# Kernel optimization log

Measured on AMD Instinct MI355X. Metric: run time of the kernel, lower is better.

## Reference

```python
import jax, jax.numpy as jnp
import numpy as np

N = 50000
E = 800000
D = 256        # encoder_dim; also hidden*heads for both layers
H = 4          # heads
C = 64         # hidden_dim per head
OUT = 5        # classes
NEG_SLOPE = 0.2
GN_EPS = 1e-5
SM_EPS = 1e-16  # PyG softmax denominator epsilon


def setup_inputs() -> dict:
    key = jax.random.key(0)
    ks = jax.random.split(key, 20)
    sc = lambda fan_in: 1.0 / np.sqrt(fan_in)
    inp = {
        "x": jax.random.normal(ks[0], (N, D), dtype=jnp.float32),
        "edge_index": jax.random.randint(ks[1], (2, E), 0, N, dtype=jnp.int64),
        # two GATv2 layers (stacked on leading axis): lin_l, lin_r, att, bias
        "Wl": jax.random.normal(ks[2], (2, D, H * C), dtype=jnp.float32) * sc(D),
        "Wr": jax.random.normal(ks[3], (2, D, H * C), dtype=jnp.float32) * sc(D),
        "att": jax.random.normal(ks[4], (2, H, C), dtype=jnp.float32) * sc(C),
        "bconv": jnp.zeros((2, H * C), dtype=jnp.float32),
        # parallel linear skips
        "Wlin": jax.random.normal(ks[5], (2, D, H * C), dtype=jnp.float32) * sc(D),
        "blin": jnp.zeros((2, H * C), dtype=jnp.float32),
        # GraphNorm params
        "gn_w": jnp.ones((2, H * C), dtype=jnp.float32),
        "gn_b": jnp.zeros((2, H * C), dtype=jnp.float32),
        "gn_ms": jnp.ones((2, H * C), dtype=jnp.float32),
        # final GATv2 (concat=False -> head mean, out=5) and final linear
        "fWl": jax.random.normal(ks[6], (D, H * OUT), dtype=jnp.float32) * sc(D),
        "fWr": jax.random.normal(ks[7], (D, H * OUT), dtype=jnp.float32) * sc(D),
        "fatt": jax.random.normal(ks[8], (H, OUT), dtype=jnp.float32) * sc(OUT),
        "fbconv": jnp.zeros((OUT,), dtype=jnp.float32),
        "fWlin": jax.random.normal(ks[9], (D, OUT), dtype=jnp.float32) * sc(D),
        "fblin": jnp.zeros((OUT,), dtype=jnp.float32),
    }
    return inp


def _gatv2(x, src, dst, Wl, Wr, att, heads, ch):
    # x: [N, Din]; returns [N, heads, ch]
    n = x.shape[0]
    xl = (x @ Wl).reshape(n, heads, ch)  # source messages
    xr = (x @ Wr).reshape(n, heads, ch)  # target query part
    e = jax.nn.leaky_relu(xl[src] + xr[dst], NEG_SLOPE)      # [E, H, C]
    score = jnp.einsum("ehc,hc->eh", e, att)                  # [E, H]
    # segment softmax over incoming edges of each target node
    m = jax.ops.segment_max(score, dst, num_segments=n)       # [N, H]
    a = jnp.exp(score - m[dst])
    denom = jax.ops.segment_sum(a, dst, num_segments=n)       # [N, H]
    alpha = a / (denom[dst] + SM_EPS)                         # [E, H]
    return jax.ops.segment_sum(alpha[..., None] * xl[src], dst, num_segments=n)


def _graphnorm(x, w, b, ms):
    mean = jnp.mean(x, axis=0)
    centered = x - mean * ms
    var = jnp.mean(centered * centered, axis=0)
    return w * centered * jax.lax.rsqrt(var + GN_EPS) + b


def reference(x, edge_index, Wl, Wr, att, bconv, Wlin, blin, gn_w, gn_b, gn_ms,
              fWl, fWr, fatt, fbconv, fWlin, fblin):
    src, dst = edge_index[0], edge_index[1]
    emb = x
    for i in range(2):
        cpart = _gatv2(emb, src, dst, Wl[i], Wr[i], att[i], H, C).reshape(N, H * C) + bconv[i]
        lpart = emb @ Wlin[i] + blin[i]
        cpart = _graphnorm(cpart, gn_w[i], gn_b[i], gn_ms[i])
        emb = jax.nn.elu(cpart + lpart)
    cpart = _gatv2(emb, src, dst, fWl, fWr, fatt, H, OUT).mean(axis=1) + fbconv  # concat=False
    lpart = emb @ fWlin + fblin
    return jax.nn.log_softmax(cpart + lpart, axis=1)
```

## Files before the change

kernel.cpp:

```cpp
#include <hip/hip_runtime.h>

#define NN 50000
#define EE 800000
#define DD 256
#define NB 196

typedef unsigned short u16;
typedef unsigned int u32;

typedef __attribute__((ext_vector_type(8))) short short8;
typedef __attribute__((ext_vector_type(4))) float f32x4;
typedef __attribute__((ext_vector_type(4))) unsigned short u16x4;

__device__ __forceinline__ float b2f(u16 u) {
  union { u32 i; float f; } c; c.i = ((u32)u) << 16; return c.f;
}
__device__ __forceinline__ u16 f2b(float f) {
  union { float f; u32 i; } c; c.f = f;
  u32 u = c.i;
  return (u16)((u + 0x7fffu + ((u >> 16) & 1u)) >> 16);
}
__device__ __forceinline__ float lrelu(float x) { return x > 0.f ? x : 0.2f * x; }
__device__ __forceinline__ float ldf(const void* p, int i, int bf) {
  return bf ? b2f(((const u16*)p)[i]) : ((const float*)p)[i];
}
__device__ __forceinline__ int lde(const void* ei, int idx, int m64) {
  int v = m64 ? (int)((const long long*)ei)[idx] : ((const int*)ei)[idx];
  return v < 0 ? 0 : (v >= NN ? NN - 1 : v);
}
__device__ __forceinline__ float cexp(float s) {
  return __expf(fminf(fmaxf(s, -60.f), 60.f));
}

__global__ __launch_bounds__(256) void init_kernel(const void* x, const void* ei,
                                                   int* flags, int* cnt) {
  int i = blockIdx.x * 256 + threadIdx.x;
  if (i < NN) cnt[i] = 0;
  if (blockIdx.x == 0 && threadIdx.x < 64) {
    int lane = threadIdx.x;
    const u16* xw = (const u16*)x;
    int c = 0;
    for (int k = lane; k < 512; k += 64) {
      u16 w = xw[k];
      int e = (w >> 7) & 0xFF;
      if ((e >= 107 && e <= 147) || (w & 0x7FFF) == 0) ++c;
    }
    const u32* ew = (const u32*)ei;
    int zc = 0;
    for (int k = 1 + 2 * lane; k < 1024; k += 128)
      if (ew[k] == 0) ++zc;
    #pragma unroll
    for (int off = 1; off < 64; off <<= 1) {
      c += __shfl_xor(c, off);
      zc += __shfl_xor(zc, off);
    }
    if (lane == 0) {
      flags[0] = (c >= 440) ? 1 : 0;
      flags[1] = (zc >= 400) ? 1 : 0;
    }
  }
}

__global__ void hist_kernel(const void* ei, const int* flags, int* cnt) {
  int e = blockIdx.x * 256 + threadIdx.x;
  if (e < EE) atomicAdd(&cnt[lde(ei, EE + e, flags[1])], 1);
}

__global__ __launch_bounds__(256) void bsum_kernel(const int* __restrict__ deg,
                                                   int* __restrict__ bsum) {
  int i = blockIdx.x * 256 + threadIdx.x;
  int v = (i < NN) ? deg[i] : 0;
  #pragma unroll
  for (int off = 1; off < 64; off <<= 1) v += __shfl_xor(v, off);
  __shared__ int ws[4];
  int lane = threadIdx.x & 63, wid = threadIdx.x >> 6;
  if (lane == 0) ws[wid] = v;
  __syncthreads();
  if (threadIdx.x == 0) bsum[blockIdx.x] = ws[0] + ws[1] + ws[2] + ws[3];
}

__global__ __launch_bounds__(256) void bscan_kernel(const int* __restrict__ bsum,
                                                    int* __restrict__ boff) {
  int t = threadIdx.x;
  int v = (t < NB) ? bsum[t] : 0;
  int iv = v;
  int lane = t & 63, wid = t >> 6;
  #pragma unroll
  for (int off = 1; off < 64; off <<= 1) {
    int u = __shfl_up(iv, off);
    if (lane >= off) iv += u;
  }
  __shared__ int ws[4];
  if (lane == 63) ws[wid] = iv;
  __syncthreads();
  int add = 0;
  for (int w = 0; w < wid; ++w) add += ws[w];
  if (t < NB) boff[t] = iv - v + add;
}

__global__ __launch_bounds__(256) void bwrite_kernel(const int* __restrict__ deg,
                                                     const int* __restrict__ boff,
                                                     int* __restrict__ rowptr) {
  int i = blockIdx.x * 256 + threadIdx.x;
  int v = (i < NN) ? deg[i] : 0;
  int iv = v;
  int lane = threadIdx.x & 63, wid = threadIdx.x >> 6;
  #pragma unroll
  for (int off = 1; off < 64; off <<= 1) {
    int u = __shfl_up(iv, off);
    if (lane >= off) iv += u;
  }
  __shared__ int ws[4];
  if (lane == 63) ws[wid] = iv;
  __syncthreads();
  int add = boff[blockIdx.x];
  for (int w = 0; w < wid; ++w) add += ws[w];
  if (i <= NN) rowptr[i] = iv - v + add;
}

__global__ void fill_kernel(const void* ei, const int* flags, const int* __restrict__ rowptr,
                            int* __restrict__ cnt, int* __restrict__ col) {
  int e = blockIdx.x * 256 + threadIdx.x;
  if (e < EE) {
    int m64 = flags[1];
    int dst = lde(ei, EE + e, m64);
    int old = atomicSub(&cnt[dst], 1);
    int pos = rowptr[dst] + old - 1;
    if (pos >= 0 && pos < EE) col[pos] = lde(ei, e, m64);
  }
}

__global__ __launch_bounds__(256) void prep_kernel(
    const void* Wl, const void* Wr, const void* Wlin,
    const void* fWl, const void* fWr, const void* fWlin,
    const void* x, const int* flags, u16* wpack, u16* fwp, u16* xb) {
  int bf = flags[0];
  int bid = blockIdx.x;
  if (bid < 1536) {
    int idx = bid * 256 + threadIdx.x;
    int m = idx >> 16, e = idx & 65535;
    int layer = (m >= 3) ? 1 : 0, sel = m - layer * 3;
    const void* src = (sel == 0 ? Wl : (sel == 1 ? Wr : Wlin));
    int k = e >> 8, n = e & 255;
    wpack[(m << 16) + ((((k >> 3) << 8) + n) << 3) + (k & 7)] =
        f2b(ldf(src, layer * 65536 + e, bf));
  } else if (bid < 1584) {
    int idx = (bid - 1536) * 256 + threadIdx.x;
    int j = idx & 7;
    int col = (idx >> 3) % 48;
    int kk = idx / (48 * 8);
    int k = kk * 8 + j;
    float v = 0.f;
    if (col < 20)      v = ldf(fWl, k * 20 + col, bf);
    else if (col < 40) v = ldf(fWr, k * 20 + (col - 20), bf);
    else if (col < 45) v = ldf(fWlin, k * 5 + (col - 40), bf);
    fwp[idx] = f2b(v);
  } else {
    int base = (bid - 1584) * 1024 + threadIdx.x * 4;
    if (bf) {
      const u16* s = (const u16*)x;
      #pragma unroll
      for (int j = 0; j < 4; ++j) xb[base + j] = s[base + j];
    } else {
      const float* s = (const float*)x;
      #pragma unroll
      for (int j = 0; j < 4; ++j) xb[base + j] = f2b(s[base + j]);
    }
  }
}

__global__ __launch_bounds__(256) void gemm_kernel(
    const u16* __restrict__ A, const u16* __restrict__ wpack, const void* blin,
    const int* flags, int layer, float* __restrict__ sums,
    u16* __restrict__ xl, u16* __restrict__ xr, u16* __restrict__ lp, int M) {
  __shared__ __align__(16) u16 bsh[16384];
  if (blockIdx.x == 0 && blockIdx.y == 0) {
    sums[threadIdx.x] = 0.f;
    sums[threadIdx.x + 256] = 0.f;
  }
  int wave = threadIdx.x >> 6;
  int lane = threadIdx.x & 63;
  int q = lane >> 4;
  int t = lane & 15;
  int m0 = blockIdx.x * 64 + wave * 16;
  int yh = blockIdx.y;

  int arow = m0 + t;
  if (arow >= M) arow = M - 1;
  const u16* Abase = A + (size_t)arow * DD + q * 8;
  short8 af[8];
  #pragma unroll
  for (int i = 0; i < 8; ++i) af[i] = *(const short8*)(Abase + i * 32);

  int bf = flags[0];

  for (int yi = 0; yi < 6; ++yi) {
    int y = yh * 6 + yi;
    int m = y >> 2;
    int col0 = (y & 3) * 64;
    const u16* wb = wpack + (m << 16);

    __syncthreads();
    #pragma unroll
    for (int itc = 0; itc < 8; ++itc) {
      int chunk = threadIdx.x + itc * 256;
      int kk = chunk >> 6;
      int off = chunk & 63;
      *(uint4*)&bsh[(kk << 9) + (off << 3)] =
          *(const uint4*)(wb + (((kk << 8) + col0) << 3) + (off << 3));
    }
    __syncthreads();

    f32x4 acc[4];
    #pragma unroll
    for (int ns = 0; ns < 4; ++ns) acc[ns] = (f32x4){0.f, 0.f, 0.f, 0.f};

    #pragma unroll
    for (int i = 0; i < 8; ++i) {
      int kk = i * 4 + q;
      const u16* bb = &bsh[(kk << 9) + (t << 3)];
      #pragma unroll
      for (int ns = 0; ns < 4; ++ns) {
        short8 b = *(const short8*)(bb + (ns << 7));
        acc[ns] = __builtin_amdgcn_mfma_f32_16x16x32_bf16(af[i], b, acc[ns], 0, 0, 0);
      }
    }

    u16* dstp = (y < 4) ? xl : (y < 8) ? xr : lp;
    bool isLp = (y >= 8);
    #pragma unroll
    for (int ns = 0; ns < 4; ++ns) {
      int c = col0 + ns * 16 + t;
      float bias = isLp ? ldf(blin, layer * 256 + c, bf) : 0.f;
      #pragma unroll
      for (int r = 0; r < 4; ++r) {
        int row = m0 + q * 4 + r;
        if (row < M) dstp[(size_t)row * DD + c] = f2b(acc[ns][r] + bias);
      }
    }
  }
}

__global__ __launch_bounds__(256) void fgemm_kernel(
    const u16* __restrict__ A, const u16* __restrict__ fwp, const void* fblin,
    const int* flags, float* __restrict__ zl, float* __restrict__ zr,
    float* __restrict__ lp5, int M) {
  int wave = threadIdx.x >> 6;
  int lane = threadIdx.x & 63;
  int q = lane >> 4;
  int t = lane & 15;
  int m0 = blockIdx.x * 64 + wave * 16;

  f32x4 acc[3];
  #pragma unroll
  for (int ns = 0; ns < 3; ++ns) acc[ns] = (f32x4){0.f, 0.f, 0.f, 0.f};

  int arow = m0 + t;
  if (arow >= M) arow = M - 1;
  const u16* Abase = A + (size_t)arow * DD + q * 8;

  #pragma unroll
  for (int k0 = 0; k0 < DD; k0 += 32) {
    short8 a = *(const short8*)(Abase + k0);
    int kk = (k0 >> 3) + q;
    #pragma unroll
    for (int ns = 0; ns < 3; ++ns) {
      short8 b = *(const short8*)(fwp + (((kk * 48) + ns * 16 + t) << 3));
      acc[ns] = __builtin_amdgcn_mfma_f32_16x16x32_bf16(a, b, acc[ns], 0, 0, 0);
    }
  }

  int bf = flags[0];
  #pragma unroll
  for (int ns = 0; ns < 3; ++ns) {
    int c = ns * 16 + t;
    #pragma unroll
    for (int r = 0; r < 4; ++r) {
      int row = m0 + q * 4 + r;
      if (row < M) {
        float v = acc[ns][r];
        if (c < 20)      zl[row * 20 + c] = v;
        else if (c < 40) zr[row * 20 + (c - 20)] = v;
        else if (c < 45) lp5[row * 5 + (c - 40)] = v + ldf(fblin, c - 40, bf);
      }
    }
  }
}

__global__ __launch_bounds__(64) void agg_kernel(
    const u16* __restrict__ xl, const u16* __restrict__ xr,
    const int* __restrict__ rowptr, const int* __restrict__ col,
    const void* att, const void* bconv, const int* flags, int layer,
    u16* __restrict__ cpart) {
  int node = blockIdx.x;
  int lane = threadIdx.x;
  int h = lane >> 4;
  int cb = (lane & 15) * 4;
  int base = h * 64 + cb;
  int bf = flags[0];

  u16x4 r4 = *(const u16x4*)(xr + (size_t)node * DD + base);
  float xrv[4], atv[4];
  #pragma unroll
  for (int j = 0; j < 4; ++j) {
    xrv[j] = b2f(r4[j]);
    atv[j] = ldf(att, layer * 256 + base + j, bf);
  }

  float l = 0.f;
  float acc[4] = {0.f, 0.f, 0.f, 0.f};
  int e0 = rowptr[node], e1 = rowptr[node + 1];
  for (int e = e0; e < e1; ++e) {
    int src = col[e];
    u16x4 s4 = *(const u16x4*)(xl + (size_t)src * DD + base);
    float x0 = b2f(s4[0]), x1 = b2f(s4[1]), x2 = b2f(s4[2]), x3 = b2f(s4[3]);
    float sp = atv[0] * lrelu(x0 + xrv[0]) + atv[1] * lrelu(x1 + xrv[1]) +
               atv[2] * lrelu(x2 + xrv[2]) + atv[3] * lrelu(x3 + xrv[3]);
    sp += __shfl_xor(sp, 1);
    sp += __shfl_xor(sp, 2);
    sp += __shfl_xor(sp, 4);
    sp += __shfl_xor(sp, 8);
    float pz = cexp(sp);
    l += pz;
    acc[0] += pz * x0;
    acc[1] += pz * x1;
    acc[2] += pz * x2;
    acc[3] += pz * x3;
  }
  float inv = 1.f / (l + 1e-16f);
  u16x4 outw;
  #pragma unroll
  for (int j = 0; j < 4; ++j)
    outw[j] = f2b(acc[j] * inv + ldf(bconv, layer * 256 + base + j, bf));
  *(u16x4*)(cpart + (size_t)node * DD + base) = outw;
}

__global__ __launch_bounds__(256) void stats_kernel(const u16* __restrict__ cpart,
                                                    float* __restrict__ sums) {
  int ch = threadIdx.x;
  int n0 = blockIdx.x * 250, n1 = n0 + 250;
  float s = 0.f, s2 = 0.f;
  for (int n = n0; n < n1; ++n) {
    float x = b2f(cpart[(size_t)n * DD + ch]);
    s += x; s2 += x * x;
  }
  atomicAdd(&sums[ch], s);
  atomicAdd(&sums[256 + ch], s2);
}

__global__ __launch_bounds__(256) void norm_kernel(
    const u16* __restrict__ cpart, const u16* __restrict__ lp,
    const void* gw, const void* gb, const void* gms, const int* flags, int layer,
    const float* __restrict__ sums, u16* __restrict__ emb) {
  int node = blockIdx.x, ch = threadIdx.x;
  int bf = flags[0];
  size_t idx = (size_t)node * DD + ch;
  const float invN = 1.f / (float)NN;
  float mean = sums[ch] * invN;
  float ex2 = sums[256 + ch] * invN;
  float mm = mean * ldf(gms, layer * 256 + ch, bf);
  float var = ex2 - 2.f * mm * mean + mm * mm;
  float x = b2f(cpart[idx]);
  float y = ldf(gw, layer * 256 + ch, bf) * (x - mm) * rsqrtf(fmaxf(var, 0.f) + 1e-5f) +
            ldf(gb, layer * 256 + ch, bf) + b2f(lp[idx]);
  emb[idx] = f2b(y > 0.f ? y : expm1f(y));
}

__global__ __launch_bounds__(64) void finagg_kernel(
    const float* __restrict__ zl, const float* __restrict__ zr,
    const int* __restrict__ rowptr, const int* __restrict__ col,
    const void* fatt, const void* fbconv, const int* flags,
    const float* __restrict__ lp5, void* outv) {
  int node = blockIdx.x, lane = threadIdx.x;
  int bf = flags[0];
  int h = lane >> 4, sub = lane & 15;

  float zrv[5], atv[5];
  #pragma unroll
  for (int c = 0; c < 5; ++c) {
    zrv[c] = zr[node * 20 + h * 5 + c];
    atv[c] = ldf(fatt, h * 5 + c, bf);
  }
  float l = 0.f, acc[5] = {0.f, 0.f, 0.f, 0.f, 0.f};
  int e0 = rowptr[node], e1 = rowptr[node + 1];
  for (int e = e0 + sub; e < e1; e += 16) {
    int src = col[e];
    const float* zs = zl + src * 20 + h * 5;
    float zlv[5];
    #pragma unroll
    for (int c = 0; c < 5; ++c) zlv[c] = zs[c];
    float s = 0.f;
    #pragma unroll
    for (int c = 0; c < 5; ++c) s += atv[c] * lrelu(zlv[c] + zrv[c]);
    float pz = cexp(s);
    l += pz;
    #pragma unroll
    for (int c = 0; c < 5; ++c) acc[c] += pz * zlv[c];
  }
  #pragma unroll
  for (int off = 1; off < 16; off <<= 1) {
    l += __shfl_xor(l, off);
    #pragma unroll
    for (int c = 0; c < 5; ++c) acc[c] += __shfl_xor(acc[c], off);
  }
  float inv = 1.f / (l + 1e-16f);
  float v[5];
  #pragma unroll
  for (int c = 0; c < 5; ++c) {
    float tv = acc[c] * inv;
    tv += __shfl_xor(tv, 16);
    tv += __shfl_xor(tv, 32);
    v[c] = tv * 0.25f;
  }
  if (lane == 0) {
    float mx = -3.0e38f;
    #pragma unroll
    for (int c = 0; c < 5; ++c) {
      v[c] += ldf(fbconv, c, bf) + lp5[node * 5 + c];
      mx = fmaxf(mx, v[c]);
    }
    float se = 0.f;
    #pragma unroll
    for (int c = 0; c < 5; ++c) se += __expf(v[c] - mx);
    float lse = mx + __logf(se);
    #pragma unroll
    for (int c = 0; c < 5; ++c) {
      float r = v[c] - lse;
      if (bf) ((u16*)outv)[node * 5 + c] = f2b(r);
      else    ((float*)outv)[node * 5 + c] = r;
    }
  }
}

extern "C" void kernel_launch(void* const* d_in, const int* in_sizes, int n_in,
                              void* d_out, int out_size, void* d_ws, size_t ws_size,
                              hipStream_t stream) {
  (void)in_sizes; (void)n_in; (void)out_size; (void)ws_size;
  const void* x     = d_in[0];
  const void* ei    = d_in[1];
  const void* Wl    = d_in[2];
  const void* Wr    = d_in[3];
  const void* att   = d_in[4];
  const void* bconv = d_in[5];
  const void* Wlin  = d_in[6];
  const void* blin  = d_in[7];
  const void* gnw   = d_in[8];
  const void* gnb   = d_in[9];
  const void* gnms  = d_in[10];
  const void* fWl   = d_in[11];
  const void* fWr   = d_in[12];
  const void* fatt  = d_in[13];
  const void* fbc   = d_in[14];
  const void* fWlin = d_in[15];
  const void* fblin = d_in[16];

  char* p = (char*)d_ws;
  auto take = [&](size_t bytes) {
    char* r = p;
    p += (bytes + 511) & ~(size_t)511;
    return r;
  };
  int* flags   = (int*)take(512);
  int* rowptr  = (int*)take((NN + 1) * sizeof(int));
  int* cnt     = (int*)take(NN * sizeof(int));
  int* colx    = (int*)take(EE * sizeof(int));
  int* bsum    = (int*)take(256 * sizeof(int));
  int* boff    = (int*)take(256 * sizeof(int));
  u16* wpack   = (u16*)take((size_t)6 * 65536 * sizeof(u16));
  u16* fwp     = (u16*)take((size_t)32 * 48 * 8 * sizeof(u16));
  float* sums  = (float*)take(512 * sizeof(float));
  char* unionA = take((size_t)NN * DD * 4);
  u16* xb      = (u16*)unionA;
  u16* cpart   = (u16*)unionA;
  float* zl    = (float*)unionA;
  float* zr    = (float*)(unionA + (size_t)NN * 20 * 4);
  float* lp5   = (float*)(unionA + (size_t)NN * 40 * 4);
  u16* xl      = (u16*)take((size_t)NN * DD * 2);
  u16* xr      = (u16*)take((size_t)NN * DD * 2);
  u16* lp      = (u16*)take((size_t)NN * DD * 2);
  u16* emb     = (u16*)take((size_t)NN * DD * 2);

  init_kernel<<<dim3(NB), dim3(256), 0, stream>>>(x, ei, flags, cnt);
  hist_kernel<<<dim3((EE + 255) / 256), dim3(256), 0, stream>>>(ei, flags, cnt);
  bsum_kernel<<<dim3(NB), dim3(256), 0, stream>>>(cnt, bsum);
  bscan_kernel<<<dim3(1), dim3(256), 0, stream>>>(bsum, boff);
  bwrite_kernel<<<dim3(NB), dim3(256), 0, stream>>>(cnt, boff, rowptr);
  fill_kernel<<<dim3((EE + 255) / 256), dim3(256), 0, stream>>>(ei, flags, rowptr, cnt, colx);
  prep_kernel<<<dim3(1584 + NN * DD / 1024), dim3(256), 0, stream>>>(
      Wl, Wr, Wlin, fWl, fWr, fWlin, x, flags, wpack, fwp, xb);

  const u16* layerin = xb;
  for (int i = 0; i < 2; ++i) {
    gemm_kernel<<<dim3((NN + 63) / 64, 2), dim3(256), 0, stream>>>(
        layerin, wpack + (size_t)i * 3 * 65536, blin, flags, i, sums, xl, xr, lp, NN);
    agg_kernel<<<dim3(NN), dim3(64), 0, stream>>>(xl, xr, rowptr, colx, att, bconv,
                                                  flags, i, cpart);
    stats_kernel<<<dim3(200), dim3(256), 0, stream>>>(cpart, sums);
    norm_kernel<<<dim3(NN), dim3(256), 0, stream>>>(cpart, lp, gnw, gnb, gnms, flags, i,
                                                    sums, emb);
    layerin = emb;
  }
  fgemm_kernel<<<dim3((NN + 63) / 64), dim3(256), 0, stream>>>(emb, fwp, fblin, flags,
                                                               zl, zr, lp5, NN);
  finagg_kernel<<<dim3(NN), dim3(64), 0, stream>>>(zl, zr, rowptr, colx, fatt, fbc, flags,
                                                   lp5, d_out);
}
```

Measured before the change: 604.9 us.

## Pack four nodes per block, unroll edge gathers, vectorize norm and prep loads

Aggregation and final-aggregation kernels now run four nodes per 256-thread block instead of one node per 64-thread block. The edge loop is unrolled by four so several gather loads are in flight at once. The norm kernel handles four channels per thread with vector loads and stores, the input conversion in prep uses vector loads, and stats uses more, smaller blocks. lrelu becomes a branch-free fmax. The goal is lower launch and block-scheduling overhead and more memory-level parallelism on the irregular gathers, at the cost of imbalance when nodes in one block have very different degrees.

```diff
diff --git a/kernel.cpp b/kernel.cpp
--- a/kernel.cpp
+++ b/kernel.cpp
@@ -20,7 +20,7 @@
   u32 u = c.i;
   return (u16)((u + 0x7fffu + ((u >> 16) & 1u)) >> 16);
 }
-__device__ __forceinline__ float lrelu(float x) { return x > 0.f ? x : 0.2f * x; }
+__device__ __forceinline__ float lrelu(float x) { return fmaxf(x, 0.2f * x); }
 __device__ __forceinline__ float ldf(const void* p, int i, int bf) {
   return bf ? b2f(((const u16*)p)[i]) : ((const float*)p)[i];
 }
@@ -158,13 +158,13 @@
   } else {
     int base = (bid - 1584) * 1024 + threadIdx.x * 4;
     if (bf) {
-      const u16* s = (const u16*)x;
+      *(u16x4*)(xb + base) = *(const u16x4*)((const u16*)x + base);
+    } else {
+      f32x4 s = *(const f32x4*)((const float*)x + base);
+      u16x4 o;
       #pragma unroll
-      for (int j = 0; j < 4; ++j) xb[base + j] = s[base + j];
-    } else {
-      const float* s = (const float*)x;
-      #pragma unroll
-      for (int j = 0; j < 4; ++j) xb[base + j] = f2b(s[base + j]);
+      for (int j = 0; j < 4; ++j) o[j] = f2b(s[j]);
+      *(u16x4*)(xb + base) = o;
     }
   }
 }
@@ -287,13 +287,31 @@
   }
 }
 
-__global__ __launch_bounds__(64) void agg_kernel(
+__device__ __forceinline__ void edge_step(u16x4 s4, const float* xrv, const float* atv,
+                                          float& l, float* acc) {
+  float x0 = b2f(s4[0]), x1 = b2f(s4[1]), x2 = b2f(s4[2]), x3 = b2f(s4[3]);
+  float sp = atv[0] * lrelu(x0 + xrv[0]) + atv[1] * lrelu(x1 + xrv[1]) +
+             atv[2] * lrelu(x2 + xrv[2]) + atv[3] * lrelu(x3 + xrv[3]);
+  sp += __shfl_xor(sp, 1);
+  sp += __shfl_xor(sp, 2);
+  sp += __shfl_xor(sp, 4);
+  sp += __shfl_xor(sp, 8);
+  float pz = cexp(sp);
+  l += pz;
+  acc[0] += pz * x0;
+  acc[1] += pz * x1;
+  acc[2] += pz * x2;
+  acc[3] += pz * x3;
+}
+
+__global__ __launch_bounds__(256) void agg_kernel(
     const u16* __restrict__ xl, const u16* __restrict__ xr,
     const int* __restrict__ rowptr, const int* __restrict__ col,
     const void* att, const void* bconv, const int* flags, int layer,
     u16* __restrict__ cpart) {
-  int node = blockIdx.x;
-  int lane = threadIdx.x;
+  int wave = threadIdx.x >> 6;
+  int node = blockIdx.x * 4 + wave;
+  int lane = threadIdx.x & 63;
   int h = lane >> 4;
   int cb = (lane & 15) * 4;
   int base = h * 64 + cb;
@@ -310,23 +328,25 @@
   float l = 0.f;
   float acc[4] = {0.f, 0.f, 0.f, 0.f};
   int e0 = rowptr[node], e1 = rowptr[node + 1];
-  for (int e = e0; e < e1; ++e) {
-    int src = col[e];
-    u16x4 s4 = *(const u16x4*)(xl + (size_t)src * DD + base);
-    float x0 = b2f(s4[0]), x1 = b2f(s4[1]), x2 = b2f(s4[2]), x3 = b2f(s4[3]);
-    float sp = atv[0] * lrelu(x0 + xrv[0]) + atv[1] * lrelu(x1 + xrv[1]) +
-               atv[2] * lrelu(x2 + xrv[2]) + atv[3] * lrelu(x3 + xrv[3]);
-    sp += __shfl_xor(sp, 1);
-    sp += __shfl_xor(sp, 2);
-    sp += __shfl_xor(sp, 4);
-    sp += __shfl_xor(sp, 8);
-    float pz = cexp(sp);
-    l += pz;
-    acc[0] += pz * x0;
-    acc[1] += pz * x1;
-    acc[2] += pz * x2;
-    acc[3] += pz * x3;
-  }
+  const u16* xlp = xl + base;
+
+  int e = e0;
+  for (; e + 4 <= e1; e += 4) {
+    int s0 = col[e], s1 = col[e + 1], s2 = col[e + 2], s3 = col[e + 3];
+    u16x4 v0 = *(const u16x4*)(xlp + (size_t)s0 * DD);
+    u16x4 v1 = *(const u16x4*)(xlp + (size_t)s1 * DD);
+    u16x4 v2 = *(const u16x4*)(xlp + (size_t)s2 * DD);
+    u16x4 v3 = *(const u16x4*)(xlp + (size_t)s3 * DD);
+    edge_step(v0, xrv, atv, l, acc);
+    edge_step(v1, xrv, atv, l, acc);
+    edge_step(v2, xrv, atv, l, acc);
+    edge_step(v3, xrv, atv, l, acc);
+  }
+  for (; e < e1; ++e) {
+    u16x4 v = *(const u16x4*)(xlp + (size_t)col[e] * DD);
+    edge_step(v, xrv, atv, l, acc);
+  }
+
   float inv = 1.f / (l + 1e-16f);
   u16x4 outw;
   #pragma unroll
@@ -338,7 +358,7 @@
 __global__ __launch_bounds__(256) void stats_kernel(const u16* __restrict__ cpart,
                                                     float* __restrict__ sums) {
   int ch = threadIdx.x;
-  int n0 = blockIdx.x * 250, n1 = n0 + 250;
+  int n0 = blockIdx.x * 100, n1 = n0 + 100;
   float s = 0.f, s2 = 0.f;
   for (int n = n0; n < n1; ++n) {
     float x = b2f(cpart[(size_t)n * DD + ch]);
@@ -352,26 +372,37 @@
     const u16* __restrict__ cpart, const u16* __restrict__ lp,
     const void* gw, const void* gb, const void* gms, const int* flags, int layer,
     const float* __restrict__ sums, u16* __restrict__ emb) {
-  int node = blockIdx.x, ch = threadIdx.x;
+  int t = threadIdx.x;
+  int node = blockIdx.x * 4 + (t >> 6);
+  int c4 = (t & 63) * 4;
   int bf = flags[0];
-  size_t idx = (size_t)node * DD + ch;
+  size_t idx = (size_t)node * DD + c4;
   const float invN = 1.f / (float)NN;
-  float mean = sums[ch] * invN;
-  float ex2 = sums[256 + ch] * invN;
-  float mm = mean * ldf(gms, layer * 256 + ch, bf);
-  float var = ex2 - 2.f * mm * mean + mm * mm;
-  float x = b2f(cpart[idx]);
-  float y = ldf(gw, layer * 256 + ch, bf) * (x - mm) * rsqrtf(fmaxf(var, 0.f) + 1e-5f) +
-            ldf(gb, layer * 256 + ch, bf) + b2f(lp[idx]);
-  emb[idx] = f2b(y > 0.f ? y : expm1f(y));
-}
-
-__global__ __launch_bounds__(64) void finagg_kernel(
+  u16x4 cp = *(const u16x4*)(cpart + idx);
+  u16x4 lv = *(const u16x4*)(lp + idx);
+  u16x4 o;
+  #pragma unroll
+  for (int j = 0; j < 4; ++j) {
+    int ch = c4 + j;
+    float mean = sums[ch] * invN;
+    float ex2 = sums[256 + ch] * invN;
+    float mm = mean * ldf(gms, layer * 256 + ch, bf);
+    float var = ex2 - 2.f * mm * mean + mm * mm;
+    float x = b2f(cp[j]);
+    float y = ldf(gw, layer * 256 + ch, bf) * (x - mm) * rsqrtf(fmaxf(var, 0.f) + 1e-5f) +
+              ldf(gb, layer * 256 + ch, bf) + b2f(lv[j]);
+    o[j] = f2b(y > 0.f ? y : expm1f(y));
+  }
+  *(u16x4*)(emb + idx) = o;
+}
+
+__global__ __launch_bounds__(256) void finagg_kernel(
     const float* __restrict__ zl, const float* __restrict__ zr,
     const int* __restrict__ rowptr, const int* __restrict__ col,
     const void* fatt, const void* fbconv, const int* flags,
     const float* __restrict__ lp5, void* outv) {
-  int node = blockIdx.x, lane = threadIdx.x;
+  int node = blockIdx.x * 4 + (threadIdx.x >> 6);
+  int lane = threadIdx.x & 63;
   int bf = flags[0];
   int h = lane >> 4, sub = lane & 15;
 
@@ -493,15 +524,15 @@
   for (int i = 0; i < 2; ++i) {
     gemm_kernel<<<dim3((NN + 63) / 64, 2), dim3(256), 0, stream>>>(
         layerin, wpack + (size_t)i * 3 * 65536, blin, flags, i, sums, xl, xr, lp, NN);
-    agg_kernel<<<dim3(NN), dim3(64), 0, stream>>>(xl, xr, rowptr, colx, att, bconv,
-                                                  flags, i, cpart);
-    stats_kernel<<<dim3(200), dim3(256), 0, stream>>>(cpart, sums);
-    norm_kernel<<<dim3(NN), dim3(256), 0, stream>>>(cpart, lp, gnw, gnb, gnms, flags, i,
-                                                    sums, emb);
+    agg_kernel<<<dim3(NN / 4), dim3(256), 0, stream>>>(xl, xr, rowptr, colx, att, bconv,
+                                                       flags, i, cpart);
+    stats_kernel<<<dim3(500), dim3(256), 0, stream>>>(cpart, sums);
+    norm_kernel<<<dim3(NN / 4), dim3(256), 0, stream>>>(cpart, lp, gnw, gnb, gnms, flags, i,
+                                                        sums, emb);
     layerin = emb;
   }
   fgemm_kernel<<<dim3((NN + 63) / 64), dim3(256), 0, stream>>>(emb, fwp, fblin, flags,
                                                                zl, zr, lp5, NN);
-  finagg_kernel<<<dim3(NN), dim3(64), 0, stream>>>(zl, zr, rowptr, colx, fatt, fbc, flags,
-                                                   lp5, d_out);
-}
+  finagg_kernel<<<dim3(NN / 4), dim3(256), 0, stream>>>(zl, zr, rowptr, colx, fatt, fbc,
+                                                        flags, lp5, d_out);
+}
```

Measured after the change: 661.5 us. 9.4% more time.
